# Performance work log

Hardware: AMD Instinct MI355X
Metric: run time of the kernel (lower is better)

The kernel has to match this reference:

```python
import jax, jax.numpy as jnp
import numpy as np

T, N, E = 8, 20000, 320000
D_IN, H, OUT = 64, 128, 2
EPS = 1e-5  # BatchNorm eps


def setup_inputs() -> dict:
    key = jax.random.key(0)
    ks = jax.random.split(key, 24)
    rn = lambda k, shape: jax.random.normal(k, shape, jnp.float32) * 0.05
    inp = {
        "x_seq": jax.random.normal(ks[0], (T, N, D_IN), jnp.float32),
        "edge_index_seq": jax.random.randint(ks[1], (T, 2, E), 0, N),
        # GCN layer 1 (D_IN -> H) + BatchNorm (eval mode: running stats)
        "W1": rn(ks[2], (D_IN, H)), "b1": jnp.zeros((H,), jnp.float32),
        "g1": jnp.ones((H,), jnp.float32), "be1": jnp.zeros((H,), jnp.float32),
        "m1": rn(ks[3], (H,)), "v1": jax.random.uniform(ks[4], (H,), jnp.float32, 0.5, 1.5),
        # GCN layer 2 (H -> H) + BatchNorm
        "W2": rn(ks[5], (H, H)), "b2": jnp.zeros((H,), jnp.float32),
        "g2": jnp.ones((H,), jnp.float32), "be2": jnp.zeros((H,), jnp.float32),
        "m2": rn(ks[6], (H,)), "v2": jax.random.uniform(ks[7], (H,), jnp.float32, 0.5, 1.5),
        # LSTM layer 0 (PyTorch layout: W_ih [4H, in], W_hh [4H, H], gate order i,f,g,o)
        "Wih0": rn(ks[8], (4 * H, H)), "Whh0": rn(ks[9], (4 * H, H)),
        "bih0": jnp.zeros((4 * H,), jnp.float32), "bhh0": jnp.zeros((4 * H,), jnp.float32),
        # LSTM layer 1
        "Wih1": rn(ks[10], (4 * H, H)), "Whh1": rn(ks[11], (4 * H, H)),
        "bih1": jnp.zeros((4 * H,), jnp.float32), "bhh1": jnp.zeros((4 * H,), jnp.float32),
        # final classifier
        "Wc": rn(ks[12], (OUT, H)), "bc": jnp.zeros((OUT,), jnp.float32),
    }
    return inp


def gcn_conv(x, src, dst, W, b):
    # GCNConv: D^{-1/2}(A+I)D^{-1/2} X W + b, self-loops added
    n = x.shape[0]
    h = x @ W                                   # [N, F_out]
    loop = jnp.arange(n)
    s = jnp.concatenate([src, loop])
    d = jnp.concatenate([dst, loop])
    deg = jax.ops.segment_sum(jnp.ones(d.shape, x.dtype), d, num_segments=n)
    dinv = jax.lax.rsqrt(deg)                   # deg >= 1 (self-loops)
    coef = dinv[s] * dinv[d]                    # [E+N]
    agg = jax.ops.segment_sum(h[s] * coef[:, None], d, num_segments=n)
    return agg + b


def batchnorm_eval(x, g, b, m, v):
    return (x - m) * jax.lax.rsqrt(v + EPS) * g + b


def lstm_layer(xs, Wih, Whh, b):
    # xs: [T, in]; returns (ys [T,H], h_T [H])
    h0 = jnp.zeros((Whh.shape[1],), xs.dtype)

    def step(carry, xt):
        h, c = carry
        gates = xt @ Wih.T + h @ Whh.T + b
        i, f, g, o = jnp.split(gates, 4, axis=-1)
        c = jax.nn.sigmoid(f) * c + jax.nn.sigmoid(i) * jnp.tanh(g)
        h = jax.nn.sigmoid(o) * jnp.tanh(c)
        return (h, c), h

    (hT, _), ys = jax.lax.scan(step, (h0, h0), xs)
    return ys, hT


def reference(x_seq, edge_index_seq, W1, b1, g1, be1, m1, v1,
              W2, b2, g2, be2, m2, v2,
              Wih0, Whh0, bih0, bhh0, Wih1, Whh1, bih1, bhh1, Wc, bc):
    def per_t(x, e):
        src, dst = e[0], e[1]
        h = gcn_conv(x, src, dst, W1, b1)
        h = jax.nn.relu(batchnorm_eval(h, g1, be1, m1, v1))
        h = gcn_conv(h, src, dst, W2, b2)
        h = batchnorm_eval(h, g2, be2, m2, v2)
        return h.mean(axis=0)                   # global mean pool (batch=None)

    emb = jax.vmap(per_t)(x_seq, edge_index_seq)  # [T, H]
    ys, _ = lstm_layer(emb, Wih0, Whh0, bih0 + bhh0)
    _, hT = lstm_layer(ys, Wih1, Whh1, bih1 + bhh1)
    out = hT @ Wc.T + bc                          # [OUT]
    return (out[None, :], hT[None, :])
```

## Files before the change

kernel.cpp:

```cpp
#include <hip/hip_runtime.h>
#include <hip/hip_fp16.h>
#include <math.h>

#define T 8
#define N 20000
#define E 320000
#define EPS 1e-5f
#define NBA 32
#define CHUNKA 10000
#define NPACK 10000
#define NPACK4 5000
#define TILES_PT 1250
#define BW 625
#define NBUK 32
#define SPAN_MAX 13824
#define CSGRID 157

typedef _Float16 f16x8 __attribute__((ext_vector_type(8)));
typedef float f32x4 __attribute__((ext_vector_type(4)));

__device__ __forceinline__ float sigm(float x) { return 1.0f / (1.0f + expf(-x)); }

__global__ __launch_bounds__(1024) void k_partA(const int* __restrict__ edges,
                                                unsigned int* __restrict__ hist_g,
                                                unsigned int* __restrict__ bpart,
                                                int* __restrict__ bcnt) {
    __shared__ unsigned int arr[CHUNKA];
    __shared__ int cnt[NBUK], cur[NBUK];
    const int t = blockIdx.x & 7, b = blockIdx.x >> 3;
    const int tid = threadIdx.x;
    const int* keys = edges + (size_t)t * 2 * E + E + b * CHUNKA;
    const int* pays = edges + (size_t)t * 2 * E + b * CHUNKA;
    for (int i = tid; i < NPACK4; i += 1024) arr[i] = 0;
    if (tid < NBUK) cnt[tid] = 0;
    __syncthreads();
    for (int i = tid; i < CHUNKA; i += 1024) {
        int k = keys[i];
        atomicAdd(&arr[k >> 2], 1u << ((k & 3) * 8));
        atomicAdd(&cnt[k / BW], 1);
    }
    __syncthreads();
    unsigned int* hout = hist_g + (size_t)(t * NBA + b) * NPACK4;
    for (int i = tid; i < NPACK4; i += 1024) hout[i] = arr[i];
    if (tid == 0) {
        int run = 0;
        for (int u = 0; u < NBUK; u++) { cur[u] = run; run += cnt[u]; }
    }
    if (tid < NBUK) bcnt[(t * NBUK + tid) * NBUK + b] = cnt[tid];
    __syncthreads();
    for (int i = tid; i < CHUNKA; i += 1024) {
        int k = keys[i];
        int p = pays[i];
        int slot = atomicAdd(&cur[k / BW], 1);
        arr[slot] = ((unsigned int)k << 15) | (unsigned int)p;
    }
    __syncthreads();
    unsigned int* outp = bpart + (size_t)(t * NBUK + b) * CHUNKA;
    for (int i = tid; i < CHUNKA; i += 1024) outp[i] = arr[i];
}

__global__ __launch_bounds__(256) void k_colsum(
    const unsigned int* __restrict__ hist_g,
    int* __restrict__ dega, float* __restrict__ dinv,
    const float* __restrict__ W1, __half* __restrict__ W1t,
    float* __restrict__ pooled) {
    const int bid = blockIdx.x, tid = threadIdx.x;
    if (bid >= CSGRID) {
        int i = (bid - CSGRID) * 256 + tid;
        int j = i & 127, k = i >> 7;
        W1t[j * 64 + k] = __float2half(W1[i]);
        if (bid == CSGRID) {
            f32x4 z = {0.f, 0.f, 0.f, 0.f};
            ((f32x4*)pooled)[tid] = z;
        }
        return;
    }
    int idx = bid * 256 + tid;
    if (idx >= T * NPACK4) return;
    int t = idx / NPACK4, i = idx - t * NPACK4;
    const unsigned int* hp = hist_g + (size_t)t * NBA * NPACK4 + i;
    unsigned int a0 = 0, a1 = 0, a2 = 0, a3 = 0;
#pragma unroll
    for (int b = 0; b < NBA; b++) {
        unsigned int h = hp[(size_t)b * NPACK4];
        a0 += h & 0xffu; a1 += (h >> 8) & 0xffu;
        a2 += (h >> 16) & 0xffu; a3 += h >> 24;
    }
    int4 dd; dd.x = (int)a0; dd.y = (int)a1; dd.z = (int)a2; dd.w = (int)a3;
    ((int4*)dega)[idx] = dd;
    float4 df;
    df.x = rsqrtf((float)a0 + 1.0f); df.y = rsqrtf((float)a1 + 1.0f);
    df.z = rsqrtf((float)a2 + 1.0f); df.w = rsqrtf((float)a3 + 1.0f);
    ((float4*)dinv)[idx] = df;
}

__global__ __launch_bounds__(1024) void k_scanN(const int* __restrict__ dega,
                                                int* __restrict__ offs) {
    const int t = blockIdx.x, tid = threadIdx.x;
    __shared__ int sh[1024];
    int local[20];
    int sum = 0;
    if (tid < 1000) {
        const int* tp = dega + t * N + tid * 20;
#pragma unroll
        for (int i = 0; i < 20; i++) { local[i] = tp[i]; sum += local[i]; }
    }
    sh[tid] = sum;
    __syncthreads();
    for (int off = 1; off < 1024; off <<= 1) {
        int v = (tid >= off) ? sh[tid - off] : 0;
        __syncthreads();
        sh[tid] += v;
        __syncthreads();
    }
    if (tid < 1000) {
        int run = t * E + sh[tid] - sum;
        int* op = offs + t * N + tid * 20;
#pragma unroll
        for (int i = 0; i < 20; i++) { op[i] = run; run += local[i]; }
    }
    if (t == T - 1 && tid == 0) offs[T * N] = T * E;
}

__global__ __launch_bounds__(1024) void k_place(const unsigned int* __restrict__ bpart,
                                                const int* __restrict__ bcnt,
                                                const int* __restrict__ offs,
                                                int* __restrict__ eidx) {
    __shared__ int stage[SPAN_MAX];
    __shared__ int cursor[BW];
    __shared__ int offb[NBUK], lenb[NBUK];
    const int t = blockIdx.x & 7, u = blockIdx.x >> 3;
    const int tid = threadIdx.x;
    const int nodeBase = t * N + u * BW;
    const int dstBase = u * BW;
    const int segStart = offs[nodeBase];
    const int segEnd = offs[nodeBase + BW];
    const int span = segEnd - segStart;
    if (tid < NBUK) {
        int s = 0;
        for (int uu = 0; uu < u; uu++) s += bcnt[(t * NBUK + uu) * NBUK + tid];
        offb[tid] = s;
        lenb[tid] = bcnt[(t * NBUK + u) * NBUK + tid];
    }
    for (int j = tid; j < BW; j += 1024) cursor[j] = offs[nodeBase + j] - segStart;
    __syncthreads();
    if (span <= SPAN_MAX) {
        for (int b = 0; b < NBUK; b++) {
            const unsigned int* src = bpart + (size_t)(t * NBUK + b) * CHUNKA + offb[b];
            int len = lenb[b];
            for (int i = tid; i < len; i += 1024) {
                unsigned int it = src[i];
                int pos = atomicAdd(&cursor[(int)(it >> 15) - dstBase], 1);
                stage[pos] = (int)(it & 0x7fffu) << 5;
            }
            __syncthreads();
        }
        int* out = eidx + segStart;
        for (int i = tid; i < span; i += 1024) out[i] = stage[i];
    } else {
        for (int b = 0; b < NBUK; b++) {
            const unsigned int* src = bpart + (size_t)(t * NBUK + b) * CHUNKA + offb[b];
            int len = lenb[b];
            for (int i = tid; i < len; i += 1024) {
                unsigned int it = src[i];
                int pos = atomicAdd(&cursor[(int)(it >> 15) - dstBase], 1);
                eidx[segStart + pos] = (int)(it & 0x7fffu) << 5;
            }
            __syncthreads();
        }
    }
}

__global__ __launch_bounds__(1024) void k_wsum(const unsigned int* __restrict__ bpart,
                                               const float* __restrict__ dinv,
                                               float* __restrict__ wpart) {
    __shared__ float wf[NPACK];
    const int t = blockIdx.x & 7, b = blockIdx.x >> 3;
    const int tid = threadIdx.x;
    const unsigned int* run = bpart + (size_t)(t * NBUK + b) * CHUNKA;
    const float* dv = dinv + t * N;
    for (int half = 0; half < 2; half++) {
        for (int i = tid; i < NPACK; i += 1024) wf[i] = 0.f;
        __syncthreads();
        int lo = half * NPACK;
        for (int i = tid; i < CHUNKA; i += 1024) {
            unsigned int it = run[i];
            int q = (int)(it & 0x7fffu) - lo;
            if (q >= 0 && q < NPACK) atomicAdd(&wf[q], dv[it >> 15]);
        }
        __syncthreads();
        float* out = wpart + (size_t)(t * NBUK + b) * N + lo;
        for (int i = tid; i < NPACK; i += 1024) out[i] = wf[i];
        __syncthreads();
    }
}

__global__ __launch_bounds__(256) void k_cvt(const float* __restrict__ x,
                                             const float* __restrict__ dinv,
                                             const float* __restrict__ wpart,
                                             float* __restrict__ alpha,
                                             __half* __restrict__ xh) {
    int idx = blockIdx.x * 256 + threadIdx.x;
    if (idx >= T * N * 16) return;
    if (idx < T * N) {
        int t = idx / N, n = idx - t * N;
        float s = 0.f;
#pragma unroll
        for (int b = 0; b < NBUK; b++) s += wpart[(size_t)(t * NBUK + b) * N + n];
        float di = dinv[idx];
        alpha[idx] = di * (s + di);
    }
    if (idx < 16) {
        ushort4 z; z.x = 0; z.y = 0; z.z = 0; z.w = 0;
        ((ushort4*)(xh + (size_t)T * N * 64))[idx] = z;
    }
    float d = dinv[idx >> 4];
    f32x4 vv = __builtin_nontemporal_load((const f32x4*)x + idx);
    __half h0 = __float2half(vv.x * d);
    __half h1 = __float2half(vv.y * d);
    __half h2 = __float2half(vv.z * d);
    __half h3 = __float2half(vv.w * d);
    ushort4 pack;
    pack.x = *(unsigned short*)&h0;
    pack.y = *(unsigned short*)&h1;
    pack.z = *(unsigned short*)&h2;
    pack.w = *(unsigned short*)&h3;
    ((ushort4*)xh)[idx] = pack;
}

__global__ __launch_bounds__(256) void k_gather(
    const int* __restrict__ eidx, const int* __restrict__ offs,
    const float* __restrict__ dinv, const __half* __restrict__ xh,
    __half* __restrict__ vh) {
    const int t = blockIdx.x & 7;
    const int n = ((blockIdx.x >> 3) << 2) + (threadIdx.x >> 6);
    const int lane = threadIdx.x & 63;
    const int f = lane & 31, g = lane >> 5;
    if (n >= N) return;
    const int node = t * N + n;
    const int start = offs[node];
    const int end = offs[node + 1];
    const __half2* xt2 = (const __half2*)(xh + (size_t)t * N * 64);
    const int zrow = (T - t) * (N * 32);
    float acc0 = 0.f, acc1 = 0.f;
    for (int bs = start; bs < end; bs += 64) {
        int cnt = end - bs; if (cnt > 64) cnt = 64;
        int idx = zrow;
        if (lane < cnt) idx = __builtin_nontemporal_load(&eidx[bs + lane]);
        __half2 hacc = __float2half2_rn(0.f);
        for (int e = 0; e < cnt; e += 16) {
            int o0 = __shfl(idx, e + 0 + g),  o1 = __shfl(idx, e + 2 + g);
            int o2 = __shfl(idx, e + 4 + g),  o3 = __shfl(idx, e + 6 + g);
            int o4 = __shfl(idx, e + 8 + g),  o5 = __shfl(idx, e + 10 + g);
            int o6 = __shfl(idx, e + 12 + g), o7 = __shfl(idx, e + 14 + g);
            __half2 u0 = xt2[o0 + f], u1 = xt2[o1 + f];
            __half2 u2 = xt2[o2 + f], u3 = xt2[o3 + f];
            __half2 u4 = xt2[o4 + f], u5 = xt2[o5 + f];
            __half2 u6 = xt2[o6 + f], u7 = xt2[o7 + f];
            __half2 s01 = __hadd2(u0, u1), s23 = __hadd2(u2, u3);
            __half2 s45 = __hadd2(u4, u5), s67 = __hadd2(u6, u7);
            __half2 s03 = __hadd2(s01, s23), s47 = __hadd2(s45, s67);
            hacc = __hadd2(hacc, __hadd2(s03, s47));
        }
        float2 fa = __half22float2(hacc);
        acc0 += fa.x;
        acc1 += fa.y;
    }
    acc0 += __shfl_down(acc0, 32);
    acc1 += __shfl_down(acc1, 32);
    if (g == 0) {
        float di = dinv[node];
        float2 us = __half22float2(xt2[(n << 5) + f]);
        float r0 = di * (acc0 + us.x);
        float r1 = di * (acc1 + us.y);
        __half2 outp = __floats2half2_rn(r0, r1);
        ((__half2*)vh)[(size_t)node * 32 + f] = outp;
    }
}

__global__ __launch_bounds__(256) void k_mfma_pool(
    const __half* __restrict__ vh, const float* __restrict__ alpha,
    const __half* __restrict__ W1t,
    const float* __restrict__ b1, const float* __restrict__ g1,
    const float* __restrict__ be1, const float* __restrict__ m1,
    const float* __restrict__ v1, float* __restrict__ pooled) {
    const int t = blockIdx.x & 7;
    const int bt = blockIdx.x >> 3;
    const int w = threadIdx.x >> 6, lane = threadIdx.x & 63;
    const int q = lane >> 4, col = lane & 15;
    const size_t tb = (size_t)t * N;

    f16x8 bfr[8][2];
    float sbv[8], stv[8];
#pragma unroll
    for (int jt = 0; jt < 8; jt++) {
        int j = jt * 16 + col;
        float s = g1[j] * rsqrtf(v1[j] + EPS);
        sbv[jt] = s;
        stv[jt] = s * b1[j] + be1[j] - m1[j] * s;
#pragma unroll
        for (int kk = 0; kk < 2; kk++)
            bfr[jt][kk] = *(const f16x8*)(W1t + (size_t)j * 64 + kk * 32 + q * 8);
    }
    float pool8[8];
#pragma unroll
    for (int jt = 0; jt < 8; jt++) pool8[jt] = 0.f;

    for (int i = 0; i < 8; i++) {
        int tau = bt * 32 + w * 8 + i;
        if (tau >= TILES_PT) break;
        int nb = tau * 16;
        const __half* vrow = vh + (tb + nb + col) * 64;
        f16x8 a0 = *(const f16x8*)(vrow + q * 8);
        f16x8 a1 = *(const f16x8*)(vrow + 32 + q * 8);
        float4 af = ((const float4*)(alpha + tb + nb))[q];
#pragma unroll
        for (int jt = 0; jt < 8; jt++) {
            f32x4 acc = {0.f, 0.f, 0.f, 0.f};
            acc = __builtin_amdgcn_mfma_f32_16x16x32_f16(a0, bfr[jt][0], acc, 0, 0, 0);
            acc = __builtin_amdgcn_mfma_f32_16x16x32_f16(a1, bfr[jt][1], acc, 0, 0, 0);
            float s = sbv[jt], sh = stv[jt];
            pool8[jt] += fmaxf(s * acc[0] + sh, 0.f) * af.x
                       + fmaxf(s * acc[1] + sh, 0.f) * af.y
                       + fmaxf(s * acc[2] + sh, 0.f) * af.z
                       + fmaxf(s * acc[3] + sh, 0.f) * af.w;
        }
    }
#pragma unroll
    for (int jt = 0; jt < 8; jt++) {
        pool8[jt] += __shfl_xor(pool8[jt], 16);
        pool8[jt] += __shfl_xor(pool8[jt], 32);
    }
    if (lane < 16) {
#pragma unroll
        for (int jt = 0; jt < 8; jt++)
            atomicAdd(&pooled[t * 128 + jt * 16 + lane], pool8[jt]);
    }
}

__global__ __launch_bounds__(512) void k_emb(
    const float* __restrict__ pooled,
    const float* __restrict__ W2, const float* __restrict__ b2,
    const float* __restrict__ g2, const float* __restrict__ be2,
    const float* __restrict__ m2, const float* __restrict__ v2,
    const float* __restrict__ Wih0, const float* __restrict__ bih0,
    const float* __restrict__ bhh0, float* __restrict__ gx0_g,
    const float* __restrict__ Whh0, const float* __restrict__ Whh1,
    const float* __restrict__ Wih1, float* __restrict__ sink) {
    const int tid = threadIdx.x;
    if (blockIdx.x >= T) {
        int bid = blockIdx.x - T;
        int start = (bid >> 3) * 24576;
        float s = 0.f;
        for (int i = start + tid; i < start + 24576; i += 512) {
            float v;
            if (i < 65536) v = Whh0[i];
            else if (i < 131072) v = Whh1[i - 65536];
            else v = Wih1[i - 131072];
            s += v;
        }
        sink[bid * 512 + tid] = s;
        return;
    }
    const int t = blockIdx.x;
    __shared__ float pm[128];
    __shared__ float es[128];
    if (tid < 128) pm[tid] = pooled[t * 128 + tid] * (1.0f / N);
    __syncthreads();
    if (tid < 128) {
        float s = g2[tid] * rsqrtf(v2[tid] + EPS);
        float sh = be2[tid] - m2[tid] * s;
        float dot = 0.f;
#pragma unroll 8
        for (int k = 0; k < 128; k++) dot += pm[k] * W2[k * 128 + tid];
        es[tid] = s * (dot + b2[tid]) + sh;
    }
    __syncthreads();
    float dot = bih0[tid] + bhh0[tid];
    const float4* w = (const float4*)(Wih0 + tid * 128);
    const float4* e4 = (const float4*)es;
#pragma unroll
    for (int k4 = 0; k4 < 32; k4++) {
        float4 a = w[k4], bb = e4[k4];
        dot += a.x * bb.x + a.y * bb.y + a.z * bb.z + a.w * bb.w;
    }
    gx0_g[t * 512 + tid] = dot;
}

__global__ __launch_bounds__(1024) void k_lstm0(
    const float* __restrict__ gx0_g, const float* __restrict__ Whh0,
    float* __restrict__ ys_g) {
    __shared__ float gx0[T][512];
    __shared__ float h[128];
    __shared__ float part[1024];
    const int tid = threadIdx.x;
    const int r = tid & 511, hf = tid >> 9;
    float4 wreg[16];
    {
        const float4* wrow = (const float4*)(Whh0 + r * 128 + hf * 64);
#pragma unroll
        for (int k = 0; k < 16; k++) wreg[k] = wrow[k];
    }
    for (int i = tid; i < T * 512; i += 1024) gx0[i >> 9][i & 511] = gx0_g[i];
    if (tid < 128) h[tid] = 0.f;
    float c = 0.f;
    __syncthreads();
    for (int t = 0; t < T; t++) {
        const float4* h4 = ((const float4*)h) + hf * 16;
        float dot = 0.f;
#pragma unroll
        for (int k = 0; k < 16; k++) {
            float4 wv = wreg[k];
            float4 hv = h4[k];
            dot += wv.x * hv.x + wv.y * hv.y + wv.z * hv.z + wv.w * hv.w;
        }
        part[tid] = dot;
        __syncthreads();
        if (tid < 128) {
            float i_ = gx0[t][tid]       + part[tid]       + part[512 + tid];
            float f_ = gx0[t][128 + tid] + part[128 + tid] + part[640 + tid];
            float g_ = gx0[t][256 + tid] + part[256 + tid] + part[768 + tid];
            float o_ = gx0[t][384 + tid] + part[384 + tid] + part[896 + tid];
            c = sigm(f_) * c + sigm(i_) * tanhf(g_);
            float hv = sigm(o_) * tanhf(c);
            h[tid] = hv;
            ys_g[t * 128 + tid] = hv;
        }
        __syncthreads();
    }
}

__global__ __launch_bounds__(1024) void k_lstm1(
    const float* __restrict__ ys_g,
    const float* __restrict__ Wih1, const float* __restrict__ bih1,
    const float* __restrict__ bhh1, const float* __restrict__ Whh1,
    const float* __restrict__ Wc, const float* __restrict__ bc,
    float* __restrict__ out) {
    __shared__ float ys[T][128];
    __shared__ float gx1h[2][T][512];
    __shared__ float h[128];
    __shared__ float part[1024];
    const int tid = threadIdx.x;
    const int r = tid & 511, hf = tid >> 9;
    float4 wreg[16];
    {
        const float4* wrow = (const float4*)(Wih1 + r * 128 + hf * 64);
#pragma unroll
        for (int k = 0; k < 16; k++) wreg[k] = wrow[k];
    }
    for (int i = tid; i < T * 128; i += 1024) ys[i >> 7][i & 127] = ys_g[i];
    __syncthreads();
    {
        float bias = (hf == 0) ? (bih1[r] + bhh1[r]) : 0.f;
        for (int t = 0; t < T; t++) {
            const float4* y4 = ((const float4*)ys[t]) + hf * 16;
            float dot = bias;
#pragma unroll
            for (int k = 0; k < 16; k++) {
                float4 wv = wreg[k];
                float4 yv = y4[k];
                dot += wv.x * yv.x + wv.y * yv.y + wv.z * yv.z + wv.w * yv.w;
            }
            gx1h[hf][t][r] = dot;
        }
    }
    {
        const float4* wrow = (const float4*)(Whh1 + r * 128 + hf * 64);
#pragma unroll
        for (int k = 0; k < 16; k++) wreg[k] = wrow[k];
    }
    if (tid < 128) h[tid] = 0.f;
    float c = 0.f;
    __syncthreads();
    for (int t = 0; t < T; t++) {
        const float4* h4 = ((const float4*)h) + hf * 16;
        float dot = 0.f;
#pragma unroll
        for (int k = 0; k < 16; k++) {
            float4 wv = wreg[k];
            float4 hv = h4[k];
            dot += wv.x * hv.x + wv.y * hv.y + wv.z * hv.z + wv.w * hv.w;
        }
        part[tid] = dot;
        __syncthreads();
        if (tid < 128) {
            float i_ = gx1h[0][t][tid]       + gx1h[1][t][tid]       + part[tid]       + part[512 + tid];
            float f_ = gx1h[0][t][128 + tid] + gx1h[1][t][128 + tid] + part[128 + tid] + part[640 + tid];
            float g_ = gx1h[0][t][256 + tid] + gx1h[1][t][256 + tid] + part[256 + tid] + part[768 + tid];
            float o_ = gx1h[0][t][384 + tid] + gx1h[1][t][384 + tid] + part[384 + tid] + part[896 + tid];
            c = sigm(f_) * c + sigm(i_) * tanhf(g_);
            h[tid] = sigm(o_) * tanhf(c);
        }
        __syncthreads();
    }
    if (tid < 2) {
        float dot = bc[tid];
#pragma unroll 8
        for (int k = 0; k < 128; k++) dot += h[k] * Wc[tid * 128 + k];
        out[tid] = dot;
    }
    if (tid < 128) out[2 + tid] = h[tid];
}

extern "C" void kernel_launch(void* const* d_in, const int* in_sizes, int n_in,
                              void* d_out, int out_size, void* d_ws, size_t ws_size,
                              hipStream_t stream) {
    const float* x    = (const float*)d_in[0];
    const int*   edges= (const int*)d_in[1];
    const float* W1   = (const float*)d_in[2];
    const float* b1   = (const float*)d_in[3];
    const float* g1   = (const float*)d_in[4];
    const float* be1  = (const float*)d_in[5];
    const float* m1   = (const float*)d_in[6];
    const float* v1   = (const float*)d_in[7];
    const float* W2   = (const float*)d_in[8];
    const float* b2   = (const float*)d_in[9];
    const float* g2   = (const float*)d_in[10];
    const float* be2  = (const float*)d_in[11];
    const float* m2   = (const float*)d_in[12];
    const float* v2   = (const float*)d_in[13];
    const float* Wih0 = (const float*)d_in[14];
    const float* Whh0 = (const float*)d_in[15];
    const float* bih0 = (const float*)d_in[16];
    const float* bhh0 = (const float*)d_in[17];
    const float* Wih1 = (const float*)d_in[18];
    const float* Whh1 = (const float*)d_in[19];
    const float* bih1 = (const float*)d_in[20];
    const float* bhh1 = (const float*)d_in[21];
    const float* Wc   = (const float*)d_in[22];
    const float* bc   = (const float*)d_in[23];

    char* base = (char*)d_ws;
    unsigned int* hist_g = (unsigned int*)base;
    unsigned int* bpart  = (unsigned int*)(base + (size_t)T * NBA * NPACK * 4);
    __half*       vh     = (__half*)base;
    char* p = base + (size_t)T * NBA * NPACK * 4 + (size_t)T * NBUK * CHUNKA * 4;
    __half* xh   = (__half*)p;              p += (size_t)T * N * 64 * 2 + 128;
    int*   offs  = (int*)p;                 p += (size_t)(T * N + 1) * 4 + 12;
    int*   dega  = (int*)p;                 p += (size_t)T * N * 4;
    float* dinv  = (float*)p;               p += (size_t)T * N * 4;
    float* alpha = (float*)p;               p += (size_t)T * N * 4;
    int*   tot   = (int*)p;                 p += (size_t)T * N * 4;
    int*   eidx  = (int*)p;                 p += (size_t)T * E * 4;
    float* wpart = (float*)p;               p += (size_t)T * NBUK * N * 4;
    int*   bcnt  = (int*)p;                 p += (size_t)T * NBUK * NBUK * 4;
    float* pooled= (float*)p;               p += (size_t)T * 128 * 4;
    float* gx0_g = (float*)p;               p += (size_t)T * 512 * 4;
    float* ys_g  = (float*)p;               p += (size_t)T * 128 * 4;
    __half* W1t  = (__half*)p;

    k_partA<<<T * NBUK, 1024, 0, stream>>>(edges, hist_g, bpart, bcnt);
    k_colsum<<<CSGRID + 32, 256, 0, stream>>>(hist_g, dega, dinv, W1, W1t, pooled);
    k_scanN<<<T, 1024, 0, stream>>>(dega, offs);
    k_place<<<T * NBUK, 1024, 0, stream>>>(bpart, bcnt, offs, eidx);
    k_wsum<<<T * NBUK, 1024, 0, stream>>>(bpart, dinv, wpart);
    k_cvt<<<(T * N * 16) / 256, 256, 0, stream>>>(x, dinv, wpart, alpha, xh);
    k_gather<<<(T * N) / 4, 256, 0, stream>>>(eidx, offs, dinv, xh, vh);
    k_mfma_pool<<<8 * 40, 256, 0, stream>>>(vh, alpha, W1t, b1, g1, be1, m1, v1, pooled);
    k_emb<<<T + 64, 512, 0, stream>>>(pooled, W2, b2, g2, be2, m2, v2, Wih0, bih0, bhh0,
                                      gx0_g, Whh0, Whh1, Wih1, (float*)tot);
    k_lstm0<<<1, 1024, 0, stream>>>(gx0_g, Whh0, ys_g);
    k_lstm1<<<1, 1024, 0, stream>>>(ys_g, Wih1, bih1, bhh1, Whh1, Wc, bc, (float*)d_out);
}
```

Before: 335.3 us.

## Fuse place/wsum/cvt kernels, fuse tail into one head kernel, widen gather loads

Merges the edge placement, weighted-degree partial sums, and fp16 conversion into one multi-role launch, and moves the alpha reduction into the MFMA pooling kernel. The embedding, both LSTM layers and the classifier now run in a single 1024-thread block alongside an L2 prefetch of the weights. The gather kernel switches to 8-byte loads with 16 lanes per row, so edge indices are scaled by 16 instead of 32. The intent is fewer kernel launches and better memory-level parallelism. The cost is extra per-tile summation over 32 partial buffers inside the pooling kernel and more serialised work in the single head block.

```diff
diff --git a/kernel.cpp b/kernel.cpp
--- a/kernel.cpp
+++ b/kernel.cpp
@@ -15,9 +15,11 @@
 #define NBUK 32
 #define SPAN_MAX 13824
 #define CSGRID 157
+#define CVTBLK 2500
 
 typedef _Float16 f16x8 __attribute__((ext_vector_type(8)));
 typedef float f32x4 __attribute__((ext_vector_type(4)));
+struct h2x2 { __half2 lo, hi; };
 
 __device__ __forceinline__ float sigm(float x) { return 1.0f / (1.0f + expf(-x)); }
 
@@ -122,15 +124,63 @@
     if (t == T - 1 && tid == 0) offs[T * N] = T * E;
 }
 
-__global__ __launch_bounds__(1024) void k_place(const unsigned int* __restrict__ bpart,
-                                                const int* __restrict__ bcnt,
-                                                const int* __restrict__ offs,
-                                                int* __restrict__ eidx) {
-    __shared__ int stage[SPAN_MAX];
+__global__ __launch_bounds__(1024) void k_pw(const unsigned int* __restrict__ bpart,
+                                             const int* __restrict__ bcnt,
+                                             const int* __restrict__ offs,
+                                             const float* __restrict__ dinv,
+                                             int* __restrict__ eidx,
+                                             float* __restrict__ wpart,
+                                             const float* __restrict__ x,
+                                             __half* __restrict__ xh) {
+    __shared__ int sbuf[SPAN_MAX];
     __shared__ int cursor[BW];
     __shared__ int offb[NBUK], lenb[NBUK];
-    const int t = blockIdx.x & 7, u = blockIdx.x >> 3;
+    const int bid = blockIdx.x;
     const int tid = threadIdx.x;
+    if (bid >= 2 * T * NBUK) {
+        int idx = (bid - 2 * T * NBUK) * 1024 + tid;
+        if (idx >= T * N * 16) return;
+        if (idx < 16) {
+            ushort4 z; z.x = 0; z.y = 0; z.z = 0; z.w = 0;
+            ((ushort4*)(xh + (size_t)T * N * 64))[idx] = z;
+        }
+        float d = dinv[idx >> 4];
+        f32x4 vv = __builtin_nontemporal_load((const f32x4*)x + idx);
+        __half h0 = __float2half(vv.x * d);
+        __half h1 = __float2half(vv.y * d);
+        __half h2 = __float2half(vv.z * d);
+        __half h3 = __float2half(vv.w * d);
+        ushort4 pack;
+        pack.x = *(unsigned short*)&h0;
+        pack.y = *(unsigned short*)&h1;
+        pack.z = *(unsigned short*)&h2;
+        pack.w = *(unsigned short*)&h3;
+        ((ushort4*)xh)[idx] = pack;
+        return;
+    }
+    if (bid >= T * NBUK) {
+        float* wf = (float*)sbuf;
+        const int bb = bid - T * NBUK;
+        const int t = bb & 7, b = bb >> 3;
+        const unsigned int* run = bpart + (size_t)(t * NBUK + b) * CHUNKA;
+        const float* dv = dinv + t * N;
+        for (int half = 0; half < 2; half++) {
+            for (int i = tid; i < NPACK; i += 1024) wf[i] = 0.f;
+            __syncthreads();
+            int lo = half * NPACK;
+            for (int i = tid; i < CHUNKA; i += 1024) {
+                unsigned int it = run[i];
+                int q = (int)(it & 0x7fffu) - lo;
+                if (q >= 0 && q < NPACK) atomicAdd(&wf[q], dv[it >> 15]);
+            }
+            __syncthreads();
+            float* out = wpart + (size_t)(t * NBUK + b) * N + lo;
+            for (int i = tid; i < NPACK; i += 1024) out[i] = wf[i];
+            __syncthreads();
+        }
+        return;
+    }
+    const int t = bid & 7, u = bid >> 3;
     const int nodeBase = t * N + u * BW;
     const int dstBase = u * BW;
     const int segStart = offs[nodeBase];
@@ -151,12 +201,12 @@
             for (int i = tid; i < len; i += 1024) {
                 unsigned int it = src[i];
                 int pos = atomicAdd(&cursor[(int)(it >> 15) - dstBase], 1);
-                stage[pos] = (int)(it & 0x7fffu) << 5;
+                sbuf[pos] = (int)(it & 0x7fffu) << 4;
             }
             __syncthreads();
         }
         int* out = eidx + segStart;
-        for (int i = tid; i < span; i += 1024) out[i] = stage[i];
+        for (int i = tid; i < span; i += 1024) out[i] = sbuf[i];
     } else {
         for (int b = 0; b < NBUK; b++) {
             const unsigned int* src = bpart + (size_t)(t * NBUK + b) * CHUNKA + offb[b];
@@ -164,68 +214,11 @@
             for (int i = tid; i < len; i += 1024) {
                 unsigned int it = src[i];
                 int pos = atomicAdd(&cursor[(int)(it >> 15) - dstBase], 1);
-                eidx[segStart + pos] = (int)(it & 0x7fffu) << 5;
-            }
-            __syncthreads();
-        }
-    }
-}
-
-__global__ __launch_bounds__(1024) void k_wsum(const unsigned int* __restrict__ bpart,
-                                               const float* __restrict__ dinv,
-                                               float* __restrict__ wpart) {
-    __shared__ float wf[NPACK];
-    const int t = blockIdx.x & 7, b = blockIdx.x >> 3;
-    const int tid = threadIdx.x;
-    const unsigned int* run = bpart + (size_t)(t * NBUK + b) * CHUNKA;
-    const float* dv = dinv + t * N;
-    for (int half = 0; half < 2; half++) {
-        for (int i = tid; i < NPACK; i += 1024) wf[i] = 0.f;
-        __syncthreads();
-        int lo = half * NPACK;
-        for (int i = tid; i < CHUNKA; i += 1024) {
-            unsigned int it = run[i];
-            int q = (int)(it & 0x7fffu) - lo;
-            if (q >= 0 && q < NPACK) atomicAdd(&wf[q], dv[it >> 15]);
-        }
-        __syncthreads();
-        float* out = wpart + (size_t)(t * NBUK + b) * N + lo;
-        for (int i = tid; i < NPACK; i += 1024) out[i] = wf[i];
-        __syncthreads();
-    }
-}
-
-__global__ __launch_bounds__(256) void k_cvt(const float* __restrict__ x,
-                                             const float* __restrict__ dinv,
-                                             const float* __restrict__ wpart,
-                                             float* __restrict__ alpha,
-                                             __half* __restrict__ xh) {
-    int idx = blockIdx.x * 256 + threadIdx.x;
-    if (idx >= T * N * 16) return;
-    if (idx < T * N) {
-        int t = idx / N, n = idx - t * N;
-        float s = 0.f;
-#pragma unroll
-        for (int b = 0; b < NBUK; b++) s += wpart[(size_t)(t * NBUK + b) * N + n];
-        float di = dinv[idx];
-        alpha[idx] = di * (s + di);
-    }
-    if (idx < 16) {
-        ushort4 z; z.x = 0; z.y = 0; z.z = 0; z.w = 0;
-        ((ushort4*)(xh + (size_t)T * N * 64))[idx] = z;
-    }
-    float d = dinv[idx >> 4];
-    f32x4 vv = __builtin_nontemporal_load((const f32x4*)x + idx);
-    __half h0 = __float2half(vv.x * d);
-    __half h1 = __float2half(vv.y * d);
-    __half h2 = __float2half(vv.z * d);
-    __half h3 = __float2half(vv.w * d);
-    ushort4 pack;
-    pack.x = *(unsigned short*)&h0;
-    pack.y = *(unsigned short*)&h1;
-    pack.z = *(unsigned short*)&h2;
-    pack.w = *(unsigned short*)&h3;
-    ((ushort4*)xh)[idx] = pack;
+                eidx[segStart + pos] = (int)(it & 0x7fffu) << 4;
+            }
+            __syncthreads();
+        }
+    }
 }
 
 __global__ __launch_bounds__(256) void k_gather(
@@ -235,52 +228,53 @@
     const int t = blockIdx.x & 7;
     const int n = ((blockIdx.x >> 3) << 2) + (threadIdx.x >> 6);
     const int lane = threadIdx.x & 63;
-    const int f = lane & 31, g = lane >> 5;
+    const int q = lane & 15, s = lane >> 4;
     if (n >= N) return;
     const int node = t * N + n;
     const int start = offs[node];
     const int end = offs[node + 1];
-    const __half2* xt2 = (const __half2*)(xh + (size_t)t * N * 64);
-    const int zrow = (T - t) * (N * 32);
-    float acc0 = 0.f, acc1 = 0.f;
+    const h2x2* xt4 = (const h2x2*)(xh + (size_t)t * N * 64);
+    const int zrow = (T - t) * (N * 16);
+    float a0 = 0.f, a1 = 0.f, a2 = 0.f, a3 = 0.f;
     for (int bs = start; bs < end; bs += 64) {
         int cnt = end - bs; if (cnt > 64) cnt = 64;
         int idx = zrow;
         if (lane < cnt) idx = __builtin_nontemporal_load(&eidx[bs + lane]);
-        __half2 hacc = __float2half2_rn(0.f);
+        __half2 hlo = __float2half2_rn(0.f);
+        __half2 hhi = __float2half2_rn(0.f);
         for (int e = 0; e < cnt; e += 16) {
-            int o0 = __shfl(idx, e + 0 + g),  o1 = __shfl(idx, e + 2 + g);
-            int o2 = __shfl(idx, e + 4 + g),  o3 = __shfl(idx, e + 6 + g);
-            int o4 = __shfl(idx, e + 8 + g),  o5 = __shfl(idx, e + 10 + g);
-            int o6 = __shfl(idx, e + 12 + g), o7 = __shfl(idx, e + 14 + g);
-            __half2 u0 = xt2[o0 + f], u1 = xt2[o1 + f];
-            __half2 u2 = xt2[o2 + f], u3 = xt2[o3 + f];
-            __half2 u4 = xt2[o4 + f], u5 = xt2[o5 + f];
-            __half2 u6 = xt2[o6 + f], u7 = xt2[o7 + f];
-            __half2 s01 = __hadd2(u0, u1), s23 = __hadd2(u2, u3);
-            __half2 s45 = __hadd2(u4, u5), s67 = __hadd2(u6, u7);
-            __half2 s03 = __hadd2(s01, s23), s47 = __hadd2(s45, s67);
-            hacc = __hadd2(hacc, __hadd2(s03, s47));
-        }
-        float2 fa = __half22float2(hacc);
-        acc0 += fa.x;
-        acc1 += fa.y;
-    }
-    acc0 += __shfl_down(acc0, 32);
-    acc1 += __shfl_down(acc1, 32);
-    if (g == 0) {
+            int o0 = __shfl(idx, e + s),      o1 = __shfl(idx, e + 4 + s);
+            int o2 = __shfl(idx, e + 8 + s),  o3 = __shfl(idx, e + 12 + s);
+            h2x2 v0 = xt4[o0 + q], v1 = xt4[o1 + q];
+            h2x2 v2 = xt4[o2 + q], v3 = xt4[o3 + q];
+            __half2 p01l = __hadd2(v0.lo, v1.lo), p23l = __hadd2(v2.lo, v3.lo);
+            __half2 p01h = __hadd2(v0.hi, v1.hi), p23h = __hadd2(v2.hi, v3.hi);
+            hlo = __hadd2(hlo, __hadd2(p01l, p23l));
+            hhi = __hadd2(hhi, __hadd2(p01h, p23h));
+        }
+        float2 flo = __half22float2(hlo), fhi = __half22float2(hhi);
+        a0 += flo.x; a1 += flo.y; a2 += fhi.x; a3 += fhi.y;
+    }
+    a0 += __shfl_xor(a0, 16); a1 += __shfl_xor(a1, 16);
+    a2 += __shfl_xor(a2, 16); a3 += __shfl_xor(a3, 16);
+    a0 += __shfl_xor(a0, 32); a1 += __shfl_xor(a1, 32);
+    a2 += __shfl_xor(a2, 32); a3 += __shfl_xor(a3, 32);
+    if (s == 0) {
         float di = dinv[node];
-        float2 us = __half22float2(xt2[(n << 5) + f]);
-        float r0 = di * (acc0 + us.x);
-        float r1 = di * (acc1 + us.y);
-        __half2 outp = __floats2half2_rn(r0, r1);
-        ((__half2*)vh)[(size_t)node * 32 + f] = outp;
+        h2x2 self = xt4[(n << 4) + q];
+        float2 sl = __half22float2(self.lo), sh = __half22float2(self.hi);
+        float r0 = di * (a0 + sl.x), r1 = di * (a1 + sl.y);
+        float r2 = di * (a2 + sh.x), r3 = di * (a3 + sh.y);
+        h2x2 outp;
+        outp.lo = __floats2half2_rn(r0, r1);
+        outp.hi = __floats2half2_rn(r2, r3);
+        ((h2x2*)vh)[(size_t)node * 16 + q] = outp;
     }
 }
 
 __global__ __launch_bounds__(256) void k_mfma_pool(
-    const __half* __restrict__ vh, const float* __restrict__ alpha,
-    const __half* __restrict__ W1t,
+    const __half* __restrict__ vh, const float* __restrict__ wpart,
+    const float* __restrict__ dinv, const __half* __restrict__ W1t,
     const float* __restrict__ b1, const float* __restrict__ g1,
     const float* __restrict__ be1, const float* __restrict__ m1,
     const float* __restrict__ v1, float* __restrict__ pooled) {
@@ -313,7 +307,18 @@
         const __half* vrow = vh + (tb + nb + col) * 64;
         f16x8 a0 = *(const f16x8*)(vrow + q * 8);
         f16x8 a1 = *(const f16x8*)(vrow + 32 + q * 8);
-        float4 af = ((const float4*)(alpha + tb + nb))[q];
+        float4 dv = ((const float4*)(dinv + tb + nb))[q];
+        float4 sv = {0.f, 0.f, 0.f, 0.f};
+#pragma unroll 8
+        for (int b = 0; b < NBUK; b++) {
+            float4 wv = ((const float4*)(wpart + (size_t)(t * NBUK + b) * N + nb))[q];
+            sv.x += wv.x; sv.y += wv.y; sv.z += wv.z; sv.w += wv.w;
+        }
+        float4 af;
+        af.x = dv.x * (sv.x + dv.x);
+        af.y = dv.y * (sv.y + dv.y);
+        af.z = dv.z * (sv.z + dv.z);
+        af.w = dv.w * (sv.w + dv.w);
 #pragma unroll
         for (int jt = 0; jt < 8; jt++) {
             f32x4 acc = {0.f, 0.f, 0.f, 0.f};
@@ -338,160 +343,151 @@
     }
 }
 
-__global__ __launch_bounds__(512) void k_emb(
+__global__ __launch_bounds__(1024) void k_head(
     const float* __restrict__ pooled,
     const float* __restrict__ W2, const float* __restrict__ b2,
     const float* __restrict__ g2, const float* __restrict__ be2,
     const float* __restrict__ m2, const float* __restrict__ v2,
     const float* __restrict__ Wih0, const float* __restrict__ bih0,
-    const float* __restrict__ bhh0, float* __restrict__ gx0_g,
-    const float* __restrict__ Whh0, const float* __restrict__ Whh1,
-    const float* __restrict__ Wih1, float* __restrict__ sink) {
+    const float* __restrict__ bhh0, const float* __restrict__ Whh0,
+    const float* __restrict__ Wih1, const float* __restrict__ bih1,
+    const float* __restrict__ bhh1, const float* __restrict__ Whh1,
+    const float* __restrict__ Wc, const float* __restrict__ bc,
+    float* __restrict__ out, float* __restrict__ sink) {
     const int tid = threadIdx.x;
-    if (blockIdx.x >= T) {
-        int bid = blockIdx.x - T;
-        int start = (bid >> 3) * 24576;
+    if (blockIdx.x > 0) {
+        int bid = blockIdx.x - 1;
+        int start = (bid >> 3) * 32768;
         float s = 0.f;
-        for (int i = start + tid; i < start + 24576; i += 512) {
+        for (int i = start + tid; i < start + 32768; i += 1024) {
             float v;
             if (i < 65536) v = Whh0[i];
             else if (i < 131072) v = Whh1[i - 65536];
-            else v = Wih1[i - 131072];
+            else if (i < 196608) v = Wih1[i - 131072];
+            else v = Wih0[i - 196608];
             s += v;
         }
-        sink[bid * 512 + tid] = s;
+        sink[bid * 1024 + tid] = s;
         return;
     }
-    const int t = blockIdx.x;
-    __shared__ float pm[128];
-    __shared__ float es[128];
-    if (tid < 128) pm[tid] = pooled[t * 128 + tid] * (1.0f / N);
-    __syncthreads();
-    if (tid < 128) {
-        float s = g2[tid] * rsqrtf(v2[tid] + EPS);
-        float sh = be2[tid] - m2[tid] * s;
+    __shared__ float es[T][128];
+    __shared__ float gx[T][512];
+    __shared__ float ys[T][128];
+    __shared__ float h[128];
+    __shared__ float part[1024];
+    const int r = tid & 511, hf = tid >> 9;
+    float c = 0.f;
+    part[tid] = pooled[tid] * (1.0f / N);
+    __syncthreads();
+    {
+        int tt = tid >> 7, j = tid & 127;
+        float sc = g2[j] * rsqrtf(v2[j] + EPS);
+        float sh = be2[j] - m2[j] * sc;
+        const float* pm = &part[tt * 128];
         float dot = 0.f;
 #pragma unroll 8
-        for (int k = 0; k < 128; k++) dot += pm[k] * W2[k * 128 + tid];
-        es[tid] = s * (dot + b2[tid]) + sh;
-    }
-    __syncthreads();
-    float dot = bih0[tid] + bhh0[tid];
-    const float4* w = (const float4*)(Wih0 + tid * 128);
-    const float4* e4 = (const float4*)es;
-#pragma unroll
-    for (int k4 = 0; k4 < 32; k4++) {
-        float4 a = w[k4], bb = e4[k4];
-        dot += a.x * bb.x + a.y * bb.y + a.z * bb.z + a.w * bb.w;
-    }
-    gx0_g[t * 512 + tid] = dot;
-}
-
-__global__ __launch_bounds__(1024) void k_lstm0(
-    const float* __restrict__ gx0_g, const float* __restrict__ Whh0,
-    float* __restrict__ ys_g) {
-    __shared__ float gx0[T][512];
-    __shared__ float h[128];
-    __shared__ float part[1024];
-    const int tid = threadIdx.x;
-    const int r = tid & 511, hf = tid >> 9;
-    float4 wreg[16];
+        for (int k = 0; k < 128; k++) dot += pm[k] * W2[k * 128 + j];
+        es[tt][j] = sc * (dot + b2[j]) + sh;
+    }
+    __syncthreads();
     {
+        float4 wreg[16];
+        const float4* wrow = (const float4*)(Wih0 + r * 128 + hf * 64);
+#pragma unroll
+        for (int k = 0; k < 16; k++) wreg[k] = wrow[k];
+        float bias = (hf == 0) ? (bih0[r] + bhh0[r]) : 0.f;
+        for (int t = 0; t < T; t++) {
+            const float4* e4 = ((const float4*)es[t]) + hf * 16;
+            float dot = bias;
+#pragma unroll
+            for (int k = 0; k < 16; k++) {
+                float4 wv = wreg[k], ev = e4[k];
+                dot += wv.x * ev.x + wv.y * ev.y + wv.z * ev.z + wv.w * ev.w;
+            }
+            part[tid] = dot;
+            __syncthreads();
+            if (tid < 512) gx[t][tid] = part[tid] + part[512 + tid];
+            __syncthreads();
+        }
+    }
+    if (tid < 128) h[tid] = 0.f;
+    __syncthreads();
+    {
+        float4 wreg[16];
         const float4* wrow = (const float4*)(Whh0 + r * 128 + hf * 64);
 #pragma unroll
         for (int k = 0; k < 16; k++) wreg[k] = wrow[k];
-    }
-    for (int i = tid; i < T * 512; i += 1024) gx0[i >> 9][i & 511] = gx0_g[i];
-    if (tid < 128) h[tid] = 0.f;
-    float c = 0.f;
-    __syncthreads();
-    for (int t = 0; t < T; t++) {
-        const float4* h4 = ((const float4*)h) + hf * 16;
-        float dot = 0.f;
-#pragma unroll
-        for (int k = 0; k < 16; k++) {
-            float4 wv = wreg[k];
-            float4 hv = h4[k];
-            dot += wv.x * hv.x + wv.y * hv.y + wv.z * hv.z + wv.w * hv.w;
-        }
-        part[tid] = dot;
-        __syncthreads();
-        if (tid < 128) {
-            float i_ = gx0[t][tid]       + part[tid]       + part[512 + tid];
-            float f_ = gx0[t][128 + tid] + part[128 + tid] + part[640 + tid];
-            float g_ = gx0[t][256 + tid] + part[256 + tid] + part[768 + tid];
-            float o_ = gx0[t][384 + tid] + part[384 + tid] + part[896 + tid];
-            c = sigm(f_) * c + sigm(i_) * tanhf(g_);
-            float hv = sigm(o_) * tanhf(c);
-            h[tid] = hv;
-            ys_g[t * 128 + tid] = hv;
-        }
-        __syncthreads();
-    }
-}
-
-__global__ __launch_bounds__(1024) void k_lstm1(
-    const float* __restrict__ ys_g,
-    const float* __restrict__ Wih1, const float* __restrict__ bih1,
-    const float* __restrict__ bhh1, const float* __restrict__ Whh1,
-    const float* __restrict__ Wc, const float* __restrict__ bc,
-    float* __restrict__ out) {
-    __shared__ float ys[T][128];
-    __shared__ float gx1h[2][T][512];
-    __shared__ float h[128];
-    __shared__ float part[1024];
-    const int tid = threadIdx.x;
-    const int r = tid & 511, hf = tid >> 9;
-    float4 wreg[16];
+        for (int t = 0; t < T; t++) {
+            const float4* h4 = ((const float4*)h) + hf * 16;
+            float dot = 0.f;
+#pragma unroll
+            for (int k = 0; k < 16; k++) {
+                float4 wv = wreg[k], hv = h4[k];
+                dot += wv.x * hv.x + wv.y * hv.y + wv.z * hv.z + wv.w * hv.w;
+            }
+            part[tid] = dot;
+            __syncthreads();
+            if (tid < 128) {
+                float i_ = gx[t][tid]       + part[tid]       + part[512 + tid];
+                float f_ = gx[t][128 + tid] + part[128 + tid] + part[640 + tid];
+                float g_ = gx[t][256 + tid] + part[256 + tid] + part[768 + tid];
+                float o_ = gx[t][384 + tid] + part[384 + tid] + part[896 + tid];
+                c = sigm(f_) * c + sigm(i_) * tanhf(g_);
+                float hv = sigm(o_) * tanhf(c);
+                h[tid] = hv;
+                ys[t][tid] = hv;
+            }
+            __syncthreads();
+        }
+    }
     {
+        float4 wreg[16];
         const float4* wrow = (const float4*)(Wih1 + r * 128 + hf * 64);
 #pragma unroll
         for (int k = 0; k < 16; k++) wreg[k] = wrow[k];
-    }
-    for (int i = tid; i < T * 128; i += 1024) ys[i >> 7][i & 127] = ys_g[i];
-    __syncthreads();
-    {
         float bias = (hf == 0) ? (bih1[r] + bhh1[r]) : 0.f;
         for (int t = 0; t < T; t++) {
             const float4* y4 = ((const float4*)ys[t]) + hf * 16;
             float dot = bias;
 #pragma unroll
             for (int k = 0; k < 16; k++) {
-                float4 wv = wreg[k];
-                float4 yv = y4[k];
+                float4 wv = wreg[k], yv = y4[k];
                 dot += wv.x * yv.x + wv.y * yv.y + wv.z * yv.z + wv.w * yv.w;
             }
-            gx1h[hf][t][r] = dot;
-        }
-    }
+            part[tid] = dot;
+            __syncthreads();
+            if (tid < 512) gx[t][tid] = part[tid] + part[512 + tid];
+            __syncthreads();
+        }
+    }
+    if (tid < 128) h[tid] = 0.f;
+    c = 0.f;
+    __syncthreads();
     {
+        float4 wreg[16];
         const float4* wrow = (const float4*)(Whh1 + r * 128 + hf * 64);
 #pragma unroll
         for (int k = 0; k < 16; k++) wreg[k] = wrow[k];
-    }
-    if (tid < 128) h[tid] = 0.f;
-    float c = 0.f;
-    __syncthreads();
-    for (int t = 0; t < T; t++) {
-        const float4* h4 = ((const float4*)h) + hf * 16;
-        float dot = 0.f;
-#pragma unroll
-        for (int k = 0; k < 16; k++) {
-            float4 wv = wreg[k];
-            float4 hv = h4[k];
-            dot += wv.x * hv.x + wv.y * hv.y + wv.z * hv.z + wv.w * hv.w;
-        }
-        part[tid] = dot;
-        __syncthreads();
-        if (tid < 128) {
-            float i_ = gx1h[0][t][tid]       + gx1h[1][t][tid]       + part[tid]       + part[512 + tid];
-            float f_ = gx1h[0][t][128 + tid] + gx1h[1][t][128 + tid] + part[128 + tid] + part[640 + tid];
-            float g_ = gx1h[0][t][256 + tid] + gx1h[1][t][256 + tid] + part[256 + tid] + part[768 + tid];
-            float o_ = gx1h[0][t][384 + tid] + gx1h[1][t][384 + tid] + part[384 + tid] + part[896 + tid];
-            c = sigm(f_) * c + sigm(i_) * tanhf(g_);
-            h[tid] = sigm(o_) * tanhf(c);
-        }
-        __syncthreads();
+        for (int t = 0; t < T; t++) {
+            const float4* h4 = ((const float4*)h) + hf * 16;
+            float dot = 0.f;
+#pragma unroll
+            for (int k = 0; k < 16; k++) {
+                float4 wv = wreg[k], hv = h4[k];
+                dot += wv.x * hv.x + wv.y * hv.y + wv.z * hv.z + wv.w * hv.w;
+            }
+            part[tid] = dot;
+            __syncthreads();
+            if (tid < 128) {
+                float i_ = gx[t][tid]       + part[tid]       + part[512 + tid];
+                float f_ = gx[t][128 + tid] + part[128 + tid] + part[640 + tid];
+                float g_ = gx[t][256 + tid] + part[256 + tid] + part[768 + tid];
+                float o_ = gx[t][384 + tid] + part[384 + tid] + part[896 + tid];
+                c = sigm(f_) * c + sigm(i_) * tanhf(g_);
+                h[tid] = sigm(o_) * tanhf(c);
+            }
+            __syncthreads();
+        }
     }
     if (tid < 2) {
         float dot = bc[tid];
@@ -539,26 +535,23 @@
     int*   offs  = (int*)p;                 p += (size_t)(T * N + 1) * 4 + 12;
     int*   dega  = (int*)p;                 p += (size_t)T * N * 4;
     float* dinv  = (float*)p;               p += (size_t)T * N * 4;
-    float* alpha = (float*)p;               p += (size_t)T * N * 4;
-    int*   tot   = (int*)p;                 p += (size_t)T * N * 4;
+    float* spare = (float*)p;               p += (size_t)T * N * 4;
+    float* sink  = (float*)p;               p += (size_t)T * N * 4;
     int*   eidx  = (int*)p;                 p += (size_t)T * E * 4;
     float* wpart = (float*)p;               p += (size_t)T * NBUK * N * 4;
     int*   bcnt  = (int*)p;                 p += (size_t)T * NBUK * NBUK * 4;
     float* pooled= (float*)p;               p += (size_t)T * 128 * 4;
-    float* gx0_g = (float*)p;               p += (size_t)T * 512 * 4;
-    float* ys_g  = (float*)p;               p += (size_t)T * 128 * 4;
     __half* W1t  = (__half*)p;
+    (void)spare;
 
     k_partA<<<T * NBUK, 1024, 0, stream>>>(edges, hist_g, bpart, bcnt);
     k_colsum<<<CSGRID + 32, 256, 0, stream>>>(hist_g, dega, dinv, W1, W1t, pooled);
     k_scanN<<<T, 1024, 0, stream>>>(dega, offs);
-    k_place<<<T * NBUK, 1024, 0, stream>>>(bpart, bcnt, offs, eidx);
-    k_wsum<<<T * NBUK, 1024, 0, stream>>>(bpart, dinv, wpart);
-    k_cvt<<<(T * N * 16) / 256, 256, 0, stream>>>(x, dinv, wpart, alpha, xh);
+    k_pw<<<2 * T * NBUK + CVTBLK, 1024, 0, stream>>>(bpart, bcnt, offs, dinv,
+                                                     eidx, wpart, x, xh);
     k_gather<<<(T * N) / 4, 256, 0, stream>>>(eidx, offs, dinv, xh, vh);
-    k_mfma_pool<<<8 * 40, 256, 0, stream>>>(vh, alpha, W1t, b1, g1, be1, m1, v1, pooled);
-    k_emb<<<T + 64, 512, 0, stream>>>(pooled, W2, b2, g2, be2, m2, v2, Wih0, bih0, bhh0,
-                                      gx0_g, Whh0, Whh1, Wih1, (float*)tot);
-    k_lstm0<<<1, 1024, 0, stream>>>(gx0_g, Whh0, ys_g);
-    k_lstm1<<<1, 1024, 0, stream>>>(ys_g, Wih1, bih1, bhh1, Whh1, Wc, bc, (float*)d_out);
-}
+    k_mfma_pool<<<8 * 40, 256, 0, stream>>>(vh, wpart, dinv, W1t, b1, g1, be1, m1, v1, pooled);
+    k_head<<<65, 1024, 0, stream>>>(pooled, W2, b2, g2, be2, m2, v2,
+                                    Wih0, bih0, bhh0, Whh0, Wih1, bih1, bhh1, Whh1,
+                                    Wc, bc, (float*)d_out, sink);
+}
```

After: 364.1 us. +8.6%, slower.
